# Kernel tuning notes

Measured on AMD Instinct MI355X. Metric: run time of the kernel, lower is better.

The kernel has to match this reference:

```python
import jax, jax.numpy as jnp
import numpy as np

NUM_CLASS = 3
SCORE_THRESH = 0.1
NMS_THRESH = 0.25
PRE = 512    # NMS_PRE_MAXSIZE (reduced from 4096 for memory; same algorithm)
POST = 100   # NMS_POST_MAXSIZE
EPS = 1e-8


def _cross(a, b):
    return a[..., 0] * b[..., 1] - a[..., 1] * b[..., 0]


def _corners(box):
    # box: (7,) = (x, y, z, dx, dy, dz, heading) -> BEV corners (4,2), CCW
    x, y, dx, dy, r = box[0], box[1], box[3], box[4], box[6]
    c, s = jnp.cos(r), jnp.sin(r)
    lx = jnp.array([0.5, -0.5, -0.5, 0.5]) * dx
    ly = jnp.array([0.5, 0.5, -0.5, -0.5]) * dy
    return jnp.stack([x + lx * c - ly * s, y + lx * s + ly * c], axis=-1)


def _in_box(pts, box):
    # pts (P,2): point-in-rotated-rect test in the box frame
    px, py = pts[:, 0] - box[0], pts[:, 1] - box[1]
    c, s = jnp.cos(box[6]), jnp.sin(box[6])
    u = px * c + py * s
    v = -px * s + py * c
    return (jnp.abs(u) <= box[3] * 0.5 + 1e-5) & (jnp.abs(v) <= box[4] * 0.5 + 1e-5)


def _bev_inter_area(ba, bb):
    # Exact rotated-rect intersection area (same construction as the CUDA
    # iou3d kernel: inside corners + edge intersections, angle-sorted shoelace).
    ca, cb = _corners(ba), _corners(bb)
    pa, ra = ca, jnp.roll(ca, -1, 0) - ca       # edges of a
    pb, rb = cb, jnp.roll(cb, -1, 0) - cb       # edges of b
    d = _cross(ra[:, None, :], rb[None, :, :])  # (4,4)
    dsafe = jnp.where(jnp.abs(d) > EPS, d, 1.0)
    qp = pb[None, :, :] - pa[:, None, :]
    t = _cross(qp, rb[None, :, :]) / dsafe
    u = _cross(qp, ra[:, None, :]) / dsafe
    vi = (jnp.abs(d) > EPS) & (t >= 0.0) & (t <= 1.0) & (u >= 0.0) & (u <= 1.0)
    ip = pa[:, None, :] + t[..., None] * ra[:, None, :]  # (4,4,2)
    pts = jnp.concatenate([ca, cb, ip.reshape(16, 2)], 0)          # (24,2)
    val = jnp.concatenate([_in_box(ca, bb), _in_box(cb, ba), vi.reshape(16)], 0)
    cnt = val.sum()
    ctr = (pts * val[:, None]).sum(0) / jnp.maximum(cnt, 1)
    ang = jnp.where(val, jnp.arctan2(pts[:, 1] - ctr[1], pts[:, 0] - ctr[0]), 1e9)
    o = jnp.argsort(ang)
    ps, vs = pts[o], val[o]
    ps = jnp.where(vs[:, None], ps, ps[0])  # collapse invalid onto first valid pt
    area = 0.5 * jnp.abs(_cross(ps, jnp.roll(ps, -1, 0)).sum())
    return jnp.where(cnt >= 3, area, 0.0)


def _iou3d(ba, bb):
    inter = _bev_inter_area(ba, bb)
    zt = jnp.minimum(ba[2] + ba[5] * 0.5, bb[2] + bb[5] * 0.5)
    zb = jnp.maximum(ba[2] - ba[5] * 0.5, bb[2] - bb[5] * 0.5)
    i3 = inter * jnp.maximum(zt - zb, 0.0)
    va = ba[3] * ba[4] * ba[5]
    vb = bb[3] * bb[4] * bb[5]
    return i3 / jnp.maximum(va + vb - i3, EPS)


_iou_mat = jax.vmap(jax.vmap(_iou3d, (None, 0)), (0, None))


def _nms(scores, boxes):
    # scores (K,) sorted descending; greedy suppression in score order
    valid = scores >= SCORE_THRESH
    iou = _iou_mat(boxes, boxes)  # (K,K)

    def body(sup, inp):
        row, v, i = inp
        keep = v & jnp.logical_not(sup[i])
        sup = sup | (keep & (row > NMS_THRESH))
        return sup, keep

    K = scores.shape[0]
    _, keep = jax.lax.scan(body, jnp.zeros((K,), bool), (iou, valid, jnp.arange(K)))
    return keep


def _post_one(cls_logits, boxes):
    # multi_classes_nms path: cls_preds_normalized=False -> sigmoid
    scores = jax.nn.sigmoid(cls_logits)  # (N, NUM_CLASS)
    out_b, out_s, out_l = [], [], []
    for k in range(NUM_CLASS):
        s = jnp.where(scores[:, k] >= SCORE_THRESH, scores[:, k], -1.0)
        top_s, idx = jax.lax.top_k(s, PRE)
        b = boxes[idx]
        keep = _nms(top_s, b)
        ks = jnp.where(keep, top_s, -1.0)
        os_, oi = jax.lax.top_k(ks, POST)
        ov = os_ >= SCORE_THRESH
        out_b.append(jnp.where(ov[:, None], b[oi], 0.0))
        out_s.append(jnp.where(ov, os_, 0.0))
        out_l.append((k + 1) * ov.astype(jnp.int32))  # final_labels = k + 1
    return (jnp.concatenate(out_b, 0), jnp.concatenate(out_s, 0),
            jnp.concatenate(out_l, 0))


def setup_inputs() -> dict:
    key = jax.random.key(0)
    k1, k2 = jax.random.split(key)
    B, N = 2, 100000
    batch_cls_preds = jax.random.normal(k1, (B, N, NUM_CLASS), dtype=jnp.float32)
    u = jax.random.uniform(k2, (B, N, 7), dtype=jnp.float32)
    x = u[..., 0] * 70.0
    y = u[..., 1] * 80.0 - 40.0
    z = u[..., 2] * 2.0 - 1.0
    dx = u[..., 3] * 3.0 + 1.5
    dy = u[..., 4] * 1.5 + 1.2
    dz = u[..., 5] * 1.0 + 1.3
    r = u[..., 6] * 2.0 * np.pi - np.pi
    batch_box_preds = jnp.stack([x, y, z, dx, dy, dz, r], axis=-1)
    return {"batch_cls_preds": batch_cls_preds, "batch_box_preds": batch_box_preds}


def reference(batch_cls_preds, batch_box_preds):
    # returns per-batch padded (pred_boxes (B, 3*POST, 7), pred_scores, pred_labels);
    # invalid slots are zeroed (label 0 == no detection)
    return jax.vmap(_post_one)(batch_cls_preds, batch_box_preds)
```

## Files before the change

kernel.cpp:

```cpp
#include <hip/hip_runtime.h>
#include <cstdint>

#define NCLS 3
#define NPTS 100000
#define NB 2
#define PRE 512
#define POST 100
#define SCORE_TH 0.1f
#define NMS_TH 0.25
#define CAP 1024
#define NBINS 384
#define XBIN_SH 16
#define XBIN_OFF (0xBFC00000u >> XBIN_SH)
#define XMARG 2e-3f
#define NPROB (NB * NCLS)
#define CPB 4
#define NKB 25
#define HPB (NCLS * NBINS)
#define BUFREG 1024
#define BUFSZ (NKB * BUFREG)
#define NCELL 36


__device__ __forceinline__ uint32_t score_key(float x)
{
    double sd = 1.0 / (1.0 + exp(-(double)x));
    float s = (float)sd;
    if (!(s >= SCORE_TH)) s = -1.0f;
    uint32_t u = __float_as_uint(s);
    return (u & 0x80000000u) ? ~u : (u | 0x80000000u);
}

__device__ __forceinline__ int xbin(float x)
{
    uint32_t u = __float_as_uint(x);
    uint32_t key = (u & 0x80000000u) ? ~u : (u | 0x80000000u);
    int b = (int)(key >> XBIN_SH) - (int)XBIN_OFF;
    return b < 0 ? 0 : (b > NBINS - 1 ? NBINS - 1 : b);
}

__global__ __launch_bounds__(1024) void hist_stage_kernel(
    const float* __restrict__ cls, uint32_t* __restrict__ hist_part,
    uint32_t* __restrict__ blkcnt, unsigned long long* __restrict__ buf)
{
    __shared__ uint32_t lh[NCLS][NBINS];
    __shared__ uint32_t lcnt3[NCLS];
    const int tid = threadIdx.x;
    for (int t = tid; t < NCLS * NBINS; t += 1024) ((uint32_t*)lh)[t] = 0;
    if (tid < NCLS) lcnt3[tid] = 0;
    __syncthreads();

    const int b = blockIdx.x / NKB, kb = blockIdx.x % NKB;
    const float* base = cls + (size_t)b * NPTS * NCLS;
    #pragma unroll
    for (int c = 0; c < CPB; ++c) {
        int i = (kb * CPB + c) * 1024 + tid;
        if (i < NPTS) {
            const float* cp = base + (size_t)i * NCLS;
            #pragma unroll
            for (int k = 0; k < NCLS; ++k) {
                float x = cp[k];
                int bn = xbin(x);
                if (bn > 0) atomicAdd(&lh[k][bn], 1u);
                if (xbin(x + XMARG) >= 1) {
                    uint32_t slot = atomicAdd(&lcnt3[k], 1u);
                    if (slot < BUFREG)
                        buf[(size_t)(b * NCLS + k) * BUFSZ + kb * BUFREG + slot]
                            = ((unsigned long long)__float_as_uint(x) << 32)
                            | (uint32_t)i;
                }
            }
        }
    }
    __syncthreads();
    uint32_t* P = hist_part + (size_t)blockIdx.x * HPB;
    for (int t = tid; t < HPB; t += 1024)
        P[t] = lh[t / NBINS][t % NBINS];
    if (tid < NCLS) {
        uint32_t c = lcnt3[tid];
        blkcnt[(b * NKB + kb) * NCLS + tid] = c < BUFREG ? c : BUFREG;
    }
}

__global__ __launch_bounds__(1024) void cell_kernel(
    const float* __restrict__ boxes, const uint32_t* __restrict__ hist_part,
    const uint32_t* __restrict__ blkcnt,
    const unsigned long long* __restrict__ buf,
    uint32_t* __restrict__ cand_idx, float* __restrict__ cand_score,
    unsigned long long* __restrict__ mask)
{
    const int blk = blockIdx.x;
    const int p = blk / NCELL;
    const int b = p / NCLS, k = p % NCLS;
    int cc = blk % NCELL;
    int wi = 0;
    while (cc >= 8 - wi) { cc -= 8 - wi; ++wi; }
    const int wj = wi + cc;
    const int tid = threadIdx.x;
    const int lane = tid & 63;
    const int wv = tid >> 6;

    __shared__ unsigned long long skey[CAP];
    __shared__ uint32_t sbins[NBINS];
    __shared__ uint32_t sblk[NKB];
    __shared__ double geo[128][20];
    __shared__ float scx[128], scy[128];
    __shared__ float sczlo[128], sczhi[128], scrad[128];
    __shared__ uint32_t lcnt;

    for (int t = tid; t < 128 * 20; t += 1024) ((double*)geo)[t] = 0.0;
    if (tid < 128) {
        scx[tid] = 0.0f; scy[tid] = 0.0f;
        sczlo[tid] = 0.0f; sczhi[tid] = 0.0f; scrad[tid] = 0.0f;
    }
    if (wi == 0 && wj == 0 && tid < PRE) {
        cand_idx[p * PRE + tid] = 0;
        cand_score[p * PRE + tid] = -1.0f;
    }
    if (tid < NKB) sblk[tid] = blkcnt[(b * NKB + tid) * NCLS + k];
    if (tid == 0) lcnt = 0;
    if (tid < NBINS) {
        uint32_t s = 0;
        const uint32_t* base2 = hist_part + (size_t)(b * NKB) * HPB
                              + k * NBINS + tid;
        #pragma unroll 5
        for (int kb = 0; kb < NKB; ++kb)
            s += base2[(size_t)kb * HPB];
        sbins[tid] = s;
    }
    __syncthreads();

    int pb;
    {
        int pbw = -1;
        uint32_t carry = 0;
        #pragma unroll
        for (int c = 5; c >= 0; --c) {
            uint32_t v = sbins[c * 64 + lane];
            #pragma unroll
            for (int off = 1; off < 64; off <<= 1) {
                uint32_t o = __shfl_down(v, off);
                v += (lane + off < 64) ? o : 0u;
            }
            uint32_t full = v + carry;
            unsigned long long bal = __ballot(full >= PRE);
            if (pbw < 0 && bal)
                pbw = c * 64 + (63 - __clzll((long long)bal));
            carry += (uint32_t)__shfl((int)v, 0);
        }
        pb = pbw < 1 ? 1 : pbw;
    }

    for (int r = 0; r < NKB; ++r) {
        if (tid < (int)sblk[r]) {
            unsigned long long e = buf[(size_t)p * BUFSZ + r * BUFREG + tid];
            float x = __uint_as_float((uint32_t)(e >> 32));
            uint32_t i = (uint32_t)e;
            if (xbin(x + XMARG) >= pb) {
                uint32_t kk = score_key(x);
                uint32_t slot = atomicAdd(&lcnt, 1u);
                if (slot < CAP)
                    skey[slot] = ((unsigned long long)kk << 32)
                               | (uint32_t)(~i);
            }
        }
    }
    __syncthreads();
    const int cnt = (int)(lcnt < CAP ? lcnt : CAP);

    unsigned long long mykey = (tid < cnt) ? skey[tid] : 0ull;
    int rank = 0;
    if (tid < cnt)
        for (int j = 0; j < cnt; ++j)
            rank += (skey[j] > mykey) ? 1 : 0;

    if (tid < cnt) {
        uint32_t idx = ~((uint32_t)mykey);
        if (wi == 0 && wj == 0 && rank < PRE) {
            uint32_t ov = (uint32_t)(mykey >> 32);
            uint32_t ub = (ov & 0x80000000u) ? (ov ^ 0x80000000u) : ~ov;
            cand_idx[p * PRE + rank] = idx;
            cand_score[p * PRE + rank] = __uint_as_float(ub);
        }
        const int slotA = rank - wi * 64;
        const int slotB = rank - wj * 64;
        const bool inA = (slotA >= 0 && slotA < 64);
        const bool inB = (slotB >= 0 && slotB < 64);
        if (inA || inB) {
            const float* bp = boxes + ((size_t)b * NPTS + idx) * 7;
            double x = bp[0], y = bp[1], z = bp[2];
            double dx = bp[3], dy = bp[4], dz = bp[5], r = bp[6];
            double c = cos(r), s = sin(r);
            double hx = 0.5 * dx, hy = 0.5 * dy;
            double zlo = z - 0.5 * dz, zhi = z + 0.5 * dz;
            double rad = sqrt(hx * hx + hy * hy);
            double V[20];
            V[0] = x; V[1] = y; V[2] = c; V[3] = s; V[4] = hx; V[5] = hy;
            V[6] = zlo; V[7] = zhi; V[8] = dx * dy * dz; V[9] = rad;
            const double lxs[4] = { hx, -hx, -hx,  hx };
            const double lys[4] = { hy,  hy, -hy, -hy };
            #pragma unroll
            for (int m = 0; m < 4; ++m) {
                V[10 + m] = x + lxs[m] * c - lys[m] * s;
                V[14 + m] = y + lxs[m] * s + lys[m] * c;
            }
            if (inA) {
                #pragma unroll
                for (int m = 0; m < 20; ++m) geo[slotA][m] = V[m];
                scx[slotA] = (float)x; scy[slotA] = (float)y;
                sczlo[slotA] = (float)zlo; sczhi[slotA] = (float)zhi;
                scrad[slotA] = (float)rad;
            }
            if (inB) {
                #pragma unroll
                for (int m = 0; m < 20; ++m) geo[64 + slotB][m] = V[m];
                scx[64 + slotB] = (float)x; scy[64 + slotB] = (float)y;
                sczlo[64 + slotB] = (float)zlo; sczhi[64 + slotB] = (float)zhi;
                scrad[64 + slotB] = (float)rad;
            }
        }
    }
    __syncthreads();

    for (int rr = wv; rr < 64; rr += 16) {
        const int bi = wi * 64 + rr;
        const int j = wj * 64 + lane;

        bool surv = false;
        if (j > bi) {
            float hz = fminf(sczhi[rr], sczhi[64 + lane])
                     - fmaxf(sczlo[rr], sczlo[64 + lane]);
            if (hz > 0.0f) {
                float ddx = scx[rr] - scx[64 + lane];
                float ddy = scy[rr] - scy[64 + lane];
                float rs = scrad[rr] + scrad[64 + lane] + 0.01f;
                surv = (ddx * ddx + ddy * ddy <= rs * rs);
            }
        }
        unsigned long long sm = __ballot(surv);
        unsigned long long supw = 0ull;
        const double* A = geo[rr];

        while (sm) {
            int jb = __ffsll(sm) - 1;
            sm &= sm - 1ull;
            const double* B = geo[64 + jb];

            double hzd = fmin(A[7], B[7]) - fmax(A[6], B[6]);
            if (hzd <= 0.0) continue;
            {
                double ddx = B[0] - A[0], ddy = B[1] - A[1];
                double ca = A[2], sa = A[3], cb2 = B[2], sb2 = B[3];
                double cd = fabs(ca * cb2 + sa * sb2);
                double sd = fabs(sa * cb2 - ca * sb2);
                double pax = fabs(ddx * ca + ddy * sa);
                double pay = fabs(-ddx * sa + ddy * ca);
                double pbx = fabs(ddx * cb2 + ddy * sb2);
                double pby = fabs(-ddx * sb2 + ddy * cb2);
                if (pax > A[4] + B[4] * cd + B[5] * sd) continue;
                if (pay > A[5] + B[4] * sd + B[5] * cd) continue;
                if (pbx > B[4] + A[4] * cd + A[5] * sd) continue;
                if (pby > B[5] + A[4] * sd + A[5] * cd) continue;
                double areaA = 4.0 * A[4] * A[5], areaB = 4.0 * B[4] * B[5];
                double i3m = fmin(areaA, areaB) * hzd;
                double den = A[8] + B[8] - i3m;
                if (den < 1e-8) den = 1e-8;
                if (!(i3m / den > (double)NMS_TH)) continue;
            }

            double PX = 0.0, PY = 0.0;
            bool valid = false;
            if (lane < 8) {
                const double* S = (lane < 4) ? A : B;
                const double* O = (lane < 4) ? B : A;
                int m = lane & 3;
                PX = S[10 + m]; PY = S[14 + m];
                double rx = PX - O[0], ry = PY - O[1];
                double u =  rx * O[2] + ry * O[3];
                double v = -rx * O[3] + ry * O[2];
                valid = (fabs(u) <= O[4] + 1e-5) && (fabs(v) <= O[5] + 1e-5);
            } else if (lane < 24) {
                int e = lane - 8, m = e >> 2, nn = e & 3;
                double ax = A[10 + m], ay = A[14 + m];
                double rax = A[10 + ((m + 1) & 3)] - ax;
                double ray = A[14 + ((m + 1) & 3)] - ay;
                double bx = B[10 + nn], by = B[14 + nn];
                double rbx = B[10 + ((nn + 1) & 3)] - bx;
                double rby = B[14 + ((nn + 1) & 3)] - by;
                double d = rax * rby - ray * rbx;
                if (fabs(d) > 1e-8) {
                    double qx = bx - ax, qy = by - ay;
                    double tt = (qx * rby - qy * rbx) / d;
                    double uu = (qx * ray - qy * rax) / d;
                    valid = (tt >= 0.0 && tt <= 1.0 && uu >= 0.0 && uu <= 1.0);
                    PX = ax + tt * rax; PY = ay + tt * ray;
                }
            }
            if (!valid) { PX = 0.0; PY = 0.0; }

            unsigned long long bal = __ballot(valid);
            int cntv = __popcll(bal);
            double sx = PX, sy = PY;
            #pragma unroll
            for (int off = 16; off; off >>= 1) {
                sx += __shfl_xor(sx, off);
                sy += __shfl_xor(sy, off);
            }
            int cdiv = cntv > 0 ? cntv : 1;
            double cxc = sx / cdiv, cyc = sy / cdiv;

            double ang = valid ? atan2(PY - cyc, PX - cxc) : 1e9;
            int sidx = lane;

            #pragma unroll
            for (int kk2 = 2; kk2 <= 32; kk2 <<= 1) {
                #pragma unroll
                for (int jj = kk2 >> 1; jj > 0; jj >>= 1) {
                    double oang = __shfl_xor(ang, jj);
                    double opx  = __shfl_xor(PX, jj);
                    double opy  = __shfl_xor(PY, jj);
                    int    oidx = __shfl_xor(sidx, jj);
                    bool iLow = (lane & jj) == 0;
                    bool dirUp = (lane & kk2) == 0;
                    bool mineFirst = (ang < oang) || (ang == oang && sidx < oidx);
                    bool keepMine = (mineFirst == (iLow == dirUp));
                    if (!keepMine) { ang = oang; PX = opx; PY = opy; sidx = oidx; }
                }
            }

            double nxp = __shfl(PX, (lane + 1) & 31);
            double nyp = __shfl(PY, (lane + 1) & 31);
            double fx  = __shfl(PX, 0);
            double fy  = __shfl(PY, 0);
            bool last = (lane == cntv - 1);
            double qx = last ? fx : nxp, qy = last ? fy : nyp;
            double contrib = 0.0;
            if (lane < cntv)
                contrib = (PX - cxc) * (qy - cyc) - (PY - cyc) * (qx - cxc);
            #pragma unroll
            for (int off = 16; off; off >>= 1)
                contrib += __shfl_xor(contrib, off);
            double inter = (cntv >= 3) ? 0.5 * fabs(contrib) : 0.0;

            if (lane == 0) {
                double zt = fmin(A[7], B[7]);
                double zb = fmax(A[6], B[6]);
                double hz = zt - zb;
                bool sup = false;
                if (hz > 0.0) {
                    double i3 = inter * hz;
                    double den = A[8] + B[8] - i3;
                    if (den < 1e-8) den = 1e-8;
                    sup = (i3 / den) > (double)NMS_TH;
                }
                if (sup) supw |= 1ull << jb;
            }
        }

        if (lane == 0)
            mask[(size_t)(p * PRE + bi) * 8 + wj] = supw;
    }
}

__global__ __launch_bounds__(256) void nms_out_kernel(
    const float* __restrict__ boxes, const uint32_t* __restrict__ cand_idx,
    const float* __restrict__ cand_score,
    const unsigned long long* __restrict__ mask, float* __restrict__ out)
{
    const int p = blockIdx.x;
    const int b = p / NCLS, k = p % NCLS;
    const int tid = threadIdx.x;

    __shared__ unsigned long long smask[PRE * 8];
    __shared__ float sscore[PRE];
    __shared__ int slist[POST];
    __shared__ int scnt;

    for (int w = tid; w < PRE * 8; w += 256)
        smask[w] = mask[(size_t)p * PRE * 8 + w];
    for (int i = tid; i < PRE; i += 256)
        sscore[i] = cand_score[p * PRE + i];
    __syncthreads();

    if (tid < 64) {
        const int ln = tid;
        unsigned long long rem = 0ull;
        #pragma unroll
        for (int w = 0; w < 8; ++w) {
            unsigned long long bw = __ballot(sscore[w * 64 + ln] >= SCORE_TH);
            if (ln == w) rem = bw;
        }
        int c = 0;
        for (;;) {
            int cv = rem ? ((ln << 6) + (__ffsll(rem) - 1)) : 4096;
            int o1 = __shfl_xor(cv, 1); cv = cv < o1 ? cv : o1;
            int o2 = __shfl_xor(cv, 2); cv = cv < o2 ? cv : o2;
            int o4 = __shfl_xor(cv, 4); cv = cv < o4 ? cv : o4;
            int i = __shfl(cv, 0);
            if (i >= 4096) break;
            if (ln == 0) slist[c] = i;
            ++c;
            if (c >= POST) break;
            unsigned long long mm = (ln < 8) ? smask[i * 8 + ln] : 0ull;
            if (ln == (i >> 6)) mm |= 1ull << (i & 63);
            rem &= ~mm;
        }
        if (ln == 0) scnt = c;
    }
    __syncthreads();

    const int cnt2 = scnt;
    for (int t2 = tid; t2 < POST; t2 += 256) {
        int row = b * (NCLS * POST) + k * POST + t2;
        float* ob = out + (size_t)row * 7;
        float* os = out + (size_t)NB * NCLS * POST * 7 + row;
        float* ol = out + (size_t)NB * NCLS * POST * 7 + (size_t)NB * NCLS * POST + row;
        if (t2 < cnt2) {
            int rr = slist[t2];
            uint32_t idx = cand_idx[p * PRE + rr];
            const float* bp = boxes + ((size_t)b * NPTS + idx) * 7;
            #pragma unroll
            for (int c7 = 0; c7 < 7; ++c7) ob[c7] = bp[c7];
            *os = sscore[rr];
            *ol = (float)(k + 1);
        } else {
            #pragma unroll
            for (int c7 = 0; c7 < 7; ++c7) ob[c7] = 0.0f;
            *os = 0.0f;
            *ol = 0.0f;
        }
    }
}

extern "C" void kernel_launch(void* const* d_in, const int* in_sizes, int n_in,
                              void* d_out, int out_size, void* d_ws, size_t ws_size,
                              hipStream_t stream)
{
    (void)in_sizes; (void)n_in; (void)out_size; (void)ws_size;
    const float* cls   = (const float*)d_in[0];
    const float* boxes = (const float*)d_in[1];
    float* out = (float*)d_out;

    char* ws = (char*)d_ws;
    uint32_t* hist_part   = (uint32_t*)(ws);
    uint32_t* blkcnt      = (uint32_t*)(ws + 230400);
    unsigned long long* buf = (unsigned long long*)(ws + 231424);
    uint32_t* cand_idx    = (uint32_t*)(ws + 1460224);
    float*    cand_score  = (float*)   (ws + 1472512);
    unsigned long long* mask = (unsigned long long*)(ws + 1484800);

    hipLaunchKernelGGL(hist_stage_kernel, dim3(NB * NKB), dim3(1024), 0,
                       stream, cls, hist_part, blkcnt, buf);
    hipLaunchKernelGGL(cell_kernel, dim3(NPROB * NCELL), dim3(1024), 0,
                       stream, boxes, hist_part, blkcnt, buf,
                       cand_idx, cand_score, mask);
    hipLaunchKernelGGL(nms_out_kernel, dim3(NPROB), dim3(256), 0, stream,
                       boxes, cand_idx, cand_score, mask, out);
}
```

Before: 141.9 us.

## Run SAT prefilter per-lane and process two box pairs per wavefront

Moves the double-precision separating-axis and max-IoU prefilter from a serial per-candidate loop into a lane-parallel evaluation across all 64 columns, so only pairs that truly need the exact polygon intersection get ballotted. The exact polygon-clip and sort then run two pairs at once, one per 32-lane half of the wave64, with shuffles and counts confined to each half and the suppression words merged at the end. This cuts serial iterations of the expensive loop, at the cost of more divergent double math in the prefilter and slightly more complex lane indexing.

```diff
diff --git a/kernel.cpp b/kernel.cpp
--- a/kernel.cpp
+++ b/kernel.cpp
@@ -222,84 +222,97 @@
     }
     __syncthreads();
 
+    const int half = lane >> 5;
+    const int lane31 = lane & 31;
     for (int rr = wv; rr < 64; rr += 16) {
         const int bi = wi * 64 + rr;
-        const int j = wj * 64 + lane;
-
-        bool surv = false;
-        if (j > bi) {
-            float hz = fminf(sczhi[rr], sczhi[64 + lane])
-                     - fmaxf(sczlo[rr], sczlo[64 + lane]);
-            if (hz > 0.0f) {
-                float ddx = scx[rr] - scx[64 + lane];
-                float ddy = scy[rr] - scy[64 + lane];
-                float rs = scrad[rr] + scrad[64 + lane] + 0.01f;
-                surv = (ddx * ddx + ddy * ddy <= rs * rs);
-            }
-        }
-        unsigned long long sm = __ballot(surv);
+        const double* A = geo[rr];
+
+        bool needPoly = false;
+        {
+            const int jcol = wj * 64 + lane;
+            if (jcol > bi) {
+                float hzf = fminf(sczhi[rr], sczhi[64 + lane])
+                          - fmaxf(sczlo[rr], sczlo[64 + lane]);
+                if (hzf > 0.0f) {
+                    float ddxf = scx[rr] - scx[64 + lane];
+                    float ddyf = scy[rr] - scy[64 + lane];
+                    float rsf = scrad[rr] + scrad[64 + lane] + 0.01f;
+                    if (ddxf * ddxf + ddyf * ddyf <= rsf * rsf) {
+                        const double* B = geo[64 + lane];
+                        double hzd = fmin(A[7], B[7]) - fmax(A[6], B[6]);
+                        if (hzd > 0.0) {
+                            double ddx = B[0] - A[0], ddy = B[1] - A[1];
+                            double ca = A[2], sa = A[3];
+                            double cb2 = B[2], sb2 = B[3];
+                            double cd = fabs(ca * cb2 + sa * sb2);
+                            double sd = fabs(sa * cb2 - ca * sb2);
+                            double pax = fabs(ddx * ca + ddy * sa);
+                            double pay = fabs(-ddx * sa + ddy * ca);
+                            double pbx = fabs(ddx * cb2 + ddy * sb2);
+                            double pby = fabs(-ddx * sb2 + ddy * cb2);
+                            if (!(pax > A[4] + B[4] * cd + B[5] * sd) &&
+                                !(pay > A[5] + B[4] * sd + B[5] * cd) &&
+                                !(pbx > B[4] + A[4] * cd + A[5] * sd) &&
+                                !(pby > B[5] + A[4] * sd + A[5] * cd)) {
+                                double areaA = 4.0 * A[4] * A[5];
+                                double areaB = 4.0 * B[4] * B[5];
+                                double i3m = fmin(areaA, areaB) * hzd;
+                                double den = A[8] + B[8] - i3m;
+                                if (den < 1e-8) den = 1e-8;
+                                needPoly = (i3m / den > (double)NMS_TH);
+                            }
+                        }
+                    }
+                }
+            }
+        }
+        unsigned long long pmask = __ballot(needPoly);
         unsigned long long supw = 0ull;
-        const double* A = geo[rr];
-
-        while (sm) {
-            int jb = __ffsll(sm) - 1;
-            sm &= sm - 1ull;
-            const double* B = geo[64 + jb];
-
-            double hzd = fmin(A[7], B[7]) - fmax(A[6], B[6]);
-            if (hzd <= 0.0) continue;
-            {
-                double ddx = B[0] - A[0], ddy = B[1] - A[1];
-                double ca = A[2], sa = A[3], cb2 = B[2], sb2 = B[3];
-                double cd = fabs(ca * cb2 + sa * sb2);
-                double sd = fabs(sa * cb2 - ca * sb2);
-                double pax = fabs(ddx * ca + ddy * sa);
-                double pay = fabs(-ddx * sa + ddy * ca);
-                double pbx = fabs(ddx * cb2 + ddy * sb2);
-                double pby = fabs(-ddx * sb2 + ddy * cb2);
-                if (pax > A[4] + B[4] * cd + B[5] * sd) continue;
-                if (pay > A[5] + B[4] * sd + B[5] * cd) continue;
-                if (pbx > B[4] + A[4] * cd + A[5] * sd) continue;
-                if (pby > B[5] + A[4] * sd + A[5] * cd) continue;
-                double areaA = 4.0 * A[4] * A[5], areaB = 4.0 * B[4] * B[5];
-                double i3m = fmin(areaA, areaB) * hzd;
-                double den = A[8] + B[8] - i3m;
-                if (den < 1e-8) den = 1e-8;
-                if (!(i3m / den > (double)NMS_TH)) continue;
-            }
+
+        while (pmask) {
+            int jb0 = __ffsll(pmask) - 1;
+            unsigned long long pm1 = pmask & (pmask - 1ull);
+            int jb1 = pm1 ? (__ffsll(pm1) - 1) : -1;
+            pmask = pm1 ? (pm1 & (pm1 - 1ull)) : 0ull;
+            const int jb = half ? jb1 : jb0;
+            const bool act = jb >= 0;
+            const double* B = geo[64 + (act ? jb : 0)];
 
             double PX = 0.0, PY = 0.0;
             bool valid = false;
-            if (lane < 8) {
-                const double* S = (lane < 4) ? A : B;
-                const double* O = (lane < 4) ? B : A;
-                int m = lane & 3;
-                PX = S[10 + m]; PY = S[14 + m];
-                double rx = PX - O[0], ry = PY - O[1];
-                double u =  rx * O[2] + ry * O[3];
-                double v = -rx * O[3] + ry * O[2];
-                valid = (fabs(u) <= O[4] + 1e-5) && (fabs(v) <= O[5] + 1e-5);
-            } else if (lane < 24) {
-                int e = lane - 8, m = e >> 2, nn = e & 3;
-                double ax = A[10 + m], ay = A[14 + m];
-                double rax = A[10 + ((m + 1) & 3)] - ax;
-                double ray = A[14 + ((m + 1) & 3)] - ay;
-                double bx = B[10 + nn], by = B[14 + nn];
-                double rbx = B[10 + ((nn + 1) & 3)] - bx;
-                double rby = B[14 + ((nn + 1) & 3)] - by;
-                double d = rax * rby - ray * rbx;
-                if (fabs(d) > 1e-8) {
-                    double qx = bx - ax, qy = by - ay;
-                    double tt = (qx * rby - qy * rbx) / d;
-                    double uu = (qx * ray - qy * rax) / d;
-                    valid = (tt >= 0.0 && tt <= 1.0 && uu >= 0.0 && uu <= 1.0);
-                    PX = ax + tt * rax; PY = ay + tt * ray;
+            if (act) {
+                if (lane31 < 8) {
+                    const double* S = (lane31 < 4) ? A : B;
+                    const double* O = (lane31 < 4) ? B : A;
+                    int m = lane31 & 3;
+                    PX = S[10 + m]; PY = S[14 + m];
+                    double rx = PX - O[0], ry = PY - O[1];
+                    double u =  rx * O[2] + ry * O[3];
+                    double v = -rx * O[3] + ry * O[2];
+                    valid = (fabs(u) <= O[4] + 1e-5) && (fabs(v) <= O[5] + 1e-5);
+                } else if (lane31 < 24) {
+                    int e = lane31 - 8, m = e >> 2, nn = e & 3;
+                    double ax = A[10 + m], ay = A[14 + m];
+                    double rax = A[10 + ((m + 1) & 3)] - ax;
+                    double ray = A[14 + ((m + 1) & 3)] - ay;
+                    double bx = B[10 + nn], by = B[14 + nn];
+                    double rbx = B[10 + ((nn + 1) & 3)] - bx;
+                    double rby = B[14 + ((nn + 1) & 3)] - by;
+                    double d = rax * rby - ray * rbx;
+                    if (fabs(d) > 1e-8) {
+                        double qx = bx - ax, qy = by - ay;
+                        double tt = (qx * rby - qy * rbx) / d;
+                        double uu = (qx * ray - qy * rax) / d;
+                        valid = (tt >= 0.0 && tt <= 1.0 && uu >= 0.0 && uu <= 1.0);
+                        PX = ax + tt * rax; PY = ay + tt * ray;
+                    }
                 }
             }
             if (!valid) { PX = 0.0; PY = 0.0; }
 
             unsigned long long bal = __ballot(valid);
-            int cntv = __popcll(bal);
+            int cntv = __popc((uint32_t)(bal >> (half ? 32 : 0)));
             double sx = PX, sy = PY;
             #pragma unroll
             for (int off = 16; off; off >>= 1) {
@@ -310,7 +323,7 @@
             double cxc = sx / cdiv, cyc = sy / cdiv;
 
             double ang = valid ? atan2(PY - cyc, PX - cxc) : 1e9;
-            int sidx = lane;
+            int sidx = lane31;
 
             #pragma unroll
             for (int kk2 = 2; kk2 <= 32; kk2 <<= 1) {
@@ -320,29 +333,29 @@
                     double opx  = __shfl_xor(PX, jj);
                     double opy  = __shfl_xor(PY, jj);
                     int    oidx = __shfl_xor(sidx, jj);
-                    bool iLow = (lane & jj) == 0;
-                    bool dirUp = (lane & kk2) == 0;
+                    bool iLow = (lane31 & jj) == 0;
+                    bool dirUp = (lane31 & kk2) == 0;
                     bool mineFirst = (ang < oang) || (ang == oang && sidx < oidx);
                     bool keepMine = (mineFirst == (iLow == dirUp));
                     if (!keepMine) { ang = oang; PX = opx; PY = opy; sidx = oidx; }
                 }
             }
 
-            double nxp = __shfl(PX, (lane + 1) & 31);
-            double nyp = __shfl(PY, (lane + 1) & 31);
-            double fx  = __shfl(PX, 0);
-            double fy  = __shfl(PY, 0);
-            bool last = (lane == cntv - 1);
+            double nxp = __shfl(PX, (half << 5) | ((lane31 + 1) & 31));
+            double nyp = __shfl(PY, (half << 5) | ((lane31 + 1) & 31));
+            double fx  = __shfl(PX, half << 5);
+            double fy  = __shfl(PY, half << 5);
+            bool last = (lane31 == cntv - 1);
             double qx = last ? fx : nxp, qy = last ? fy : nyp;
             double contrib = 0.0;
-            if (lane < cntv)
+            if (lane31 < cntv)
                 contrib = (PX - cxc) * (qy - cyc) - (PY - cyc) * (qx - cxc);
             #pragma unroll
             for (int off = 16; off; off >>= 1)
                 contrib += __shfl_xor(contrib, off);
             double inter = (cntv >= 3) ? 0.5 * fabs(contrib) : 0.0;
 
-            if (lane == 0) {
+            if (act && lane31 == 0) {
                 double zt = fmin(A[7], B[7]);
                 double zb = fmax(A[6], B[6]);
                 double hz = zt - zb;
@@ -357,6 +370,7 @@
             }
         }
 
+        supw |= __shfl_xor(supw, 32);
         if (lane == 0)
             mask[(size_t)(p * PRE + bi) * 8 + wj] = supw;
     }
```

Measured after the change: 138.1 us. 2.7% less time.
